# Performance work log

Measured on AMD Instinct MI355X. Metric: run time of the kernel, lower is better.

Reference implementation:

```python
import jax, jax.numpy as jnp
import numpy as np

B, T, C = 4, 1024, 1024
H, D = 16, 64            # num_heads, head_size = C // H
F = 4096                 # ffwd_size
L = 4                    # num_layers
VOCAB = 64               # input_size (activity vocab)
OUT = 65                 # output_size (acts + 1 duration)
LEN = 1024               # positional table length (block_size)


def _rmsnorm(x, g):
    eps = jnp.finfo(x.dtype).eps
    return x * jax.lax.rsqrt(jnp.mean(x * x, axis=-1, keepdims=True) + eps) * g


def setup_inputs() -> dict:
    key = jax.random.key(0)
    ks = jax.random.split(key, 16)
    std = 0.02
    acts = jax.random.randint(ks[0], (B, T), 0, VOCAB, dtype=jnp.int32)
    durations = jax.random.uniform(ks[1], (B, T), dtype=jnp.float32)
    emb_table = jax.random.normal(ks[2], (VOCAB, C - 1), dtype=jnp.float32) * std
    pos_table = jax.random.normal(ks[3], (LEN, C), dtype=jnp.float32) * std
    Wq = jax.random.normal(ks[4], (L, H, C, D), dtype=jnp.float32) * std
    Wk = jax.random.normal(ks[5], (L, H, C, D), dtype=jnp.float32) * std
    Wv = jax.random.normal(ks[6], (L, H, C, D), dtype=jnp.float32) * std
    Wo = jax.random.normal(ks[7], (L, C, C), dtype=jnp.float32) * std
    bo = jnp.zeros((L, C), dtype=jnp.float32)
    W1 = jax.random.normal(ks[8], (L, C, F), dtype=jnp.float32) * std
    b1 = jnp.zeros((L, F), dtype=jnp.float32)
    W2 = jax.random.normal(ks[9], (L, F, C), dtype=jnp.float32) * std
    b2 = jnp.zeros((L, C), dtype=jnp.float32)
    g1 = jnp.ones((L, C), dtype=jnp.float32)
    g2 = jnp.ones((L, C), dtype=jnp.float32)
    lm_W = jax.random.normal(ks[10], (C, OUT), dtype=jnp.float32) * std
    lm_b = jnp.zeros((OUT,), dtype=jnp.float32)
    return dict(acts=acts, durations=durations, emb_table=emb_table, pos_table=pos_table,
                Wq=Wq, Wk=Wk, Wv=Wv, Wo=Wo, bo=bo, W1=W1, b1=b1, W2=W2, b2=b2,
                g1=g1, g2=g2, lm_W=lm_W, lm_b=lm_b)


def reference(acts, durations, emb_table, pos_table, Wq, Wk, Wv, Wo, bo,
              W1, b1, W2, b2, g1, g2, lm_W, lm_b):
    # embedding: concat(act embedding [C-1], duration scalar) -> [B, T, C]
    x = jnp.concatenate([emb_table[acts], durations[..., None]], axis=-1)
    x = x + pos_table[:T]
    tril = jnp.tril(jnp.ones((T, T), dtype=bool))
    scale = D ** -0.5
    for l in range(L):
        h = _rmsnorm(x, g1[l])
        q = jnp.einsum('btc,hcd->bhtd', h, Wq[l])
        k = jnp.einsum('btc,hcd->bhtd', h, Wk[l])
        v = jnp.einsum('btc,hcd->bhtd', h, Wv[l])
        wei = jnp.einsum('bhtd,bhsd->bhts', q, k) * scale
        wei = jnp.where(tril, wei, -jnp.inf)
        wei = jax.nn.softmax(wei, axis=-1)
        o = jnp.einsum('bhts,bhsd->bhtd', wei, v)           # [B, H, T, D]
        o = o.transpose(0, 2, 1, 3).reshape(B, T, H * D)     # concat heads
        x = x + o @ Wo[l] + bo[l]
        h2 = _rmsnorm(x, g2[l])
        x = x + jax.nn.gelu(h2 @ W1[l] + b1[l], approximate=False) @ W2[l] + b2[l]
    logits = x @ lm_W + lm_b
    acts_logits, dur = logits[..., :OUT - 1], logits[..., OUT - 1:]
    acts_log_probs = jax.nn.log_softmax(acts_logits, axis=-1)
    log_dur = jnp.log(jax.nn.sigmoid(dur))
    return jnp.concatenate([acts_log_probs, log_dur], axis=-1)
```

## Files before the change

kernel.cpp:

```cpp
#include <hip/hip_runtime.h>

#define Bq 4
#define Tq 1024
#define Cq 1024
#define Hq 16
#define Dq 64
#define Fq 4096
#define Lq 4
#define BT (Bq*Tq)

typedef __attribute__((ext_vector_type(8))) __bf16 bf16x8;
typedef __attribute__((ext_vector_type(4))) float  floatx4;

__device__ __forceinline__ unsigned short f2bf(float f) {
  unsigned int u = __builtin_bit_cast(unsigned int, f);
  u = (u + 0x7FFFu + ((u >> 16) & 1u)) >> 16;
  return (unsigned short)u;
}

__device__ __forceinline__ void gld_lds16(const void* g, void* lds) {
  __builtin_amdgcn_global_load_lds(
      (const __attribute__((address_space(1))) unsigned int*)g,
      (__attribute__((address_space(3))) unsigned int*)lds, 16, 0, 0);
}

__device__ __forceinline__ void barrier_vmcnt4() {
  asm volatile("s_waitcnt vmcnt(4)\n\ts_barrier" ::: "memory");
}

__global__ __launch_bounds__(256) void embed_kernel(
    const int* __restrict__ acts, const float* __restrict__ dur,
    const float* __restrict__ emb, const float* __restrict__ pos,
    float* __restrict__ x)
{
  int tok = blockIdx.x;
  int t = tok & (Tq-1);
  int a = acts[tok];
  const float* er = emb + (size_t)a * (Cq-1);
  const float* pr = pos + (size_t)t * Cq;
  float* xr = x + (size_t)tok * Cq;
  float dv = dur[tok];
  for (int c = threadIdx.x; c < Cq; c += 256) {
    float v = (c < Cq-1) ? er[c] : dv;
    xr[c] = v + pr[c];
  }
}

__global__ __launch_bounds__(256) void rmsnorm_kernel(
    const float* __restrict__ x, const float* __restrict__ g,
    unsigned short* __restrict__ h)
{
  int tok = blockIdx.x, tid = threadIdx.x;
  const float4* xr = (const float4*)(x + (size_t)tok * Cq);
  float4 v = xr[tid];
  float ss = v.x*v.x + v.y*v.y + v.z*v.z + v.w*v.w;
  #pragma unroll
  for (int s = 32; s >= 1; s >>= 1) ss += __shfl_xor(ss, s, 64);
  __shared__ float ws4[4];
  if ((tid & 63) == 0) ws4[tid >> 6] = ss;
  __syncthreads();
  float tot = ws4[0] + ws4[1] + ws4[2] + ws4[3];
  float r = rsqrtf(tot * (1.0f/(float)Cq) + 1.1920928955078125e-07f);
  float4 gv = ((const float4*)g)[tid];
  unsigned short o4[4] = { f2bf(v.x*r*gv.x), f2bf(v.y*r*gv.y),
                           f2bf(v.z*r*gv.z), f2bf(v.w*r*gv.w) };
  *(uint2*)(h + (size_t)tok*Cq + tid*4) = *(const uint2*)o4;
}

__global__ void prep_layer_kernel(
    const float* __restrict__ Wq, const float* __restrict__ Wk,
    const float* __restrict__ Wv, const float* __restrict__ Wo,
    const float* __restrict__ W1, const float* __restrict__ W2,
    unsigned short* __restrict__ wqkvl, unsigned short* __restrict__ wol,
    unsigned short* __restrict__ w1l,   unsigned short* __restrict__ w2l)
{
  __shared__ float tile[32][33];
  int z = blockIdx.x;
  const float* in; unsigned short* out;
  int R, Cc, tx, ty;
  if (z < 3072) {
    int i = z >> 10, t = z & 1023;
    int hh = t >> 6, rem = t & 63;
    ty = rem >> 1; tx = rem & 1;
    const float* w = (i == 0) ? Wq : (i == 1) ? Wk : Wv;
    in = w + (size_t)hh * Cq * Dq;
    out = wqkvl + (size_t)i * 1024 * 1024 + (size_t)hh * 64 * 1024;
    R = 1024; Cc = 64;
  } else if (z < 4096) {
    int t = z - 3072;
    tx = t & 31; ty = t >> 5;
    in = Wo; out = wol; R = 1024; Cc = 1024;
  } else if (z < 8192) {
    int t = z - 4096;
    tx = t & 127; ty = t >> 7;
    in = W1; out = w1l; R = 1024; Cc = 4096;
  } else {
    int t = z - 8192;
    tx = t & 31; ty = t >> 5;
    in = W2; out = w2l; R = 4096; Cc = 1024;
  }
  int c0 = tx * 32, r0 = ty * 32;
  int lx = threadIdx.x, ly = threadIdx.y;
  #pragma unroll
  for (int i = 0; i < 32; i += 8)
    tile[ly+i][lx] = in[(size_t)(r0+ly+i)*Cc + c0 + lx];
  __syncthreads();
  #pragma unroll
  for (int i = 0; i < 32; i += 8)
    out[(size_t)(c0+ly+i)*R + r0 + lx] = f2bf(tile[lx][ly+i]);
}

template <int EPI>
__global__ __launch_bounds__(256)
void gemm_bt_kernel(const unsigned short* __restrict__ A, int lda,
                    const unsigned short* __restrict__ Bt, int ldb,
                    int KS,
                    unsigned short* __restrict__ outB, int ldc,
                    unsigned short* __restrict__ vT,
                    float* __restrict__ outF, int ldf,
                    const float* __restrict__ bias)
{
  __shared__ unsigned short lds_a[3*4096];
  __shared__ unsigned short lds_b[3*4096];
  int tid = threadIdx.x;
  int lane = tid & 63, wv = tid >> 6;
  int lane15 = lane & 15, laneh = lane >> 4;
  int m0 = blockIdx.y * 128, n0 = blockIdx.x * 128;
  int wm = wv & 1, wn = wv >> 1;

  floatx4 acc[4][4];
  #pragma unroll
  for (int i = 0; i < 4; i++)
    #pragma unroll
    for (int j = 0; j < 4; j++) acc[i][j] = (floatx4){0.f,0.f,0.f,0.f};

  int seg0 = (wv*2+0)*64 + lane;
  int seg1 = (wv*2+1)*64 + lane;
  int ra0 = seg0 >> 2, ca0 = ((seg0 & 3) ^ (ra0 & 3)) * 8;
  int ra1 = seg1 >> 2, ca1 = ((seg1 & 3) ^ (ra1 & 3)) * 8;
  const unsigned short* a_src0 = A  + (size_t)(m0+ra0)*lda + ca0;
  const unsigned short* a_src1 = A  + (size_t)(m0+ra1)*lda + ca1;
  const unsigned short* b_src0 = Bt + (size_t)(n0+ra0)*ldb + ca0;
  const unsigned short* b_src1 = Bt + (size_t)(n0+ra1)*ldb + ca1;
  unsigned short* a_dst0 = &lds_a[(wv*2+0)*512];
  unsigned short* a_dst1 = &lds_a[(wv*2+1)*512];
  unsigned short* b_dst0 = &lds_b[(wv*2+0)*512];
  unsigned short* b_dst1 = &lds_b[(wv*2+1)*512];

  int sx = (laneh ^ (lane15 & 3)) * 8;

  int kbeg = (EPI == 3) ? blockIdx.z * KS : 0;
  int nIter = KS >> 5;

  auto stage = [&](int k0, int buf) {
    int off = buf * 4096;
    gld_lds16(a_src0 + k0, a_dst0 + off);
    gld_lds16(a_src1 + k0, a_dst1 + off);
    gld_lds16(b_src0 + k0, b_dst0 + off);
    gld_lds16(b_src1 + k0, b_dst1 + off);
  };

  stage(kbeg, 0);
  stage(kbeg + 32, 1);
  int cb = 0, pb = 2;
  for (int it = 0; it < nIter; ++it) {
    barrier_vmcnt4();
    if (it + 2 < nIter) stage(kbeg + (it+2)*32, pb);
    const unsigned short* la = &lds_a[cb*4096];
    const unsigned short* lb = &lds_b[cb*4096];
    bf16x8 af[4], bf[4];
    #pragma unroll
    for (int i = 0; i < 4; i++)
      af[i] = *(const bf16x8*)&la[(wm*64 + i*16 + lane15)*32 + sx];
    #pragma unroll
    for (int j = 0; j < 4; j++)
      bf[j] = *(const bf16x8*)&lb[(wn*64 + j*16 + lane15)*32 + sx];
    #pragma unroll
    for (int i = 0; i < 4; i++)
      #pragma unroll
      for (int j = 0; j < 4; j++)
        acc[i][j] = __builtin_amdgcn_mfma_f32_16x16x32_bf16(af[i], bf[j], acc[i][j], 0, 0, 0);
    cb = (cb == 2) ? 0 : cb + 1;
    pb = (pb == 2) ? 0 : pb + 1;
  }

  float* outFz = (EPI == 3) ? outF + (size_t)blockIdx.z * BT * Cq : outF;

  #pragma unroll
  for (int i = 0; i < 4; i++) {
    int row = m0 + wm*64 + i*16 + laneh*4;
    #pragma unroll
    for (int j = 0; j < 4; j++) {
      int col = n0 + wn*64 + j*16 + lane15;
      #pragma unroll
      for (int r = 0; r < 4; r++) {
        float v = acc[i][j][r];
        int rr = row + r;
        if constexpr (EPI == 0) {
          if (col < 2048) {
            outB[(size_t)rr*ldc + col] = f2bf(v);
          } else {
            int b = rr >> 10, t = rr & (Tq-1);
            int hd = col - 2048, hh = hd >> 6, d = hd & 63;
            vT[(((size_t)b*Hq + hh)*Dq + d)*Tq + t] = f2bf(v);
          }
        } else if constexpr (EPI == 1) {
          float z = v + bias[col];
          float u = 0.79788456080286536f * (z + 0.044715f * z*z*z);
          float t = 1.f - 2.f / (__expf(2.f*u) + 1.f);
          float gl = 0.5f * z * (1.f + t);
          outB[(size_t)rr*ldc + col] = f2bf(gl);
        } else if constexpr (EPI == 2) {
          outF[(size_t)rr*ldf + col] += v + bias[col];
        } else {
          outFz[(size_t)rr*ldf + col] = v;
        }
      }
    }
  }
}

__global__ __launch_bounds__(256) void splitk_reduce_kernel(
    const float* __restrict__ p, float* __restrict__ x,
    const float* __restrict__ bias)
{
  size_t o = ((size_t)blockIdx.x * 256 + threadIdx.x) * 4;
  float4 a = *(const float4*)(p + o);
  float4 b = *(const float4*)(p + (size_t)BT*Cq + o);
  float4 xv = *(const float4*)(x + o);
  float4 bi = *(const float4*)(bias + (o & (Cq-1)));
  xv.x += a.x + b.x + bi.x;
  xv.y += a.y + b.y + bi.y;
  xv.z += a.z + b.z + bi.z;
  xv.w += a.w + b.w + bi.w;
  *(float4*)(x + o) = xv;
}

__global__ __launch_bounds__(256)
void attn_kernel(const unsigned short* __restrict__ qk,
                 const unsigned short* __restrict__ vT,
                 unsigned short* __restrict__ ob)
{
  __shared__ unsigned short Ks [2][64*64];
  __shared__ unsigned short Vts[2][64*64];
  __shared__ unsigned short Ps [4*16*64];
  int tid = threadIdx.x, lane = tid & 63, wv = tid >> 6;
  int lane15 = lane & 15, laneh = lane >> 4;
  int blk = blockIdx.x;
  int p = blk & 7, bh = blk >> 3;
  int h = bh & (Hq-1), b = bh >> 4;
  size_t tokbase = (size_t)b * Tq;
  const unsigned short* Kbase = qk + tokbase*2048 + 1024 + h*64;
  const unsigned short* Vbase = vT + (size_t)bh * Dq * Tq;

  int so  = (laneh ^ (lane15 & 7)) * 8;
  int so32 = so ^ 32;
  unsigned short* Pw = &Ps[wv*1024];

  auto stage = [&](int j0, int buf) {
    #pragma unroll
    for (int i = 0; i < 2; i++) {
      int seg = (wv*2+i)*64 + lane;
      int row = seg >> 3;
      int col = ((seg & 7) ^ (row & 7)) * 8;
      gld_lds16(Kbase + (size_t)(j0+row)*2048 + col, &Ks [buf][(wv*2+i)*512]);
      gld_lds16(Vbase + (size_t)row*Tq + j0 + col,   &Vts[buf][(wv*2+i)*512]);
    }
  };

  for (int phase = 0; phase < 2; ++phase) {
    int qt = phase ? (15 - p) : p;
    int qrow0 = qt*64 + wv*16;
    bf16x8 qf0, qf1;
    {
      const unsigned short* qp = qk + (tokbase + qrow0 + lane15)*2048 + h*64 + laneh*8;
      qf0 = *(const bf16x8*)(qp);
      qf1 = *(const bf16x8*)(qp + 32);
    }
    floatx4 oacc[4];
    #pragma unroll
    for (int d = 0; d < 4; d++) oacc[d] = (floatx4){0.f,0.f,0.f,0.f};
    float mrow = -__builtin_inff(), lrow = 0.f;
    int nT = qt + 1;

    __syncthreads();
    stage(0, 0);
    for (int it = 0; it < nT; ++it) {
      __syncthreads();
      if (it + 1 < nT) stage((it+1)*64, (it+1) & 1);
      int buf = it & 1;
      int j0 = it*64;

      floatx4 sac[4];
      #pragma unroll
      for (int jt = 0; jt < 4; jt++) {
        int row = jt*16 + lane15;
        bf16x8 kf0 = *(const bf16x8*)&Ks[buf][row*64 + so];
        bf16x8 kf1 = *(const bf16x8*)&Ks[buf][row*64 + so32];
        sac[jt] = (floatx4){0.f,0.f,0.f,0.f};
        sac[jt] = __builtin_amdgcn_mfma_f32_16x16x32_bf16(kf0, qf0, sac[jt], 0, 0, 0);
        sac[jt] = __builtin_amdgcn_mfma_f32_16x16x32_bf16(kf1, qf1, sac[jt], 0, 0, 0);
      }
      if (j0 + 63 > qrow0) {
        int tokg = qrow0 + lane15;
        #pragma unroll
        for (int jt = 0; jt < 4; jt++)
          #pragma unroll
          for (int r = 0; r < 4; r++) {
            int kv = j0 + jt*16 + laneh*4 + r;
            sac[jt][r] = (kv <= tokg) ? sac[jt][r] * 0.125f : -__builtin_inff();
          }
      } else {
        #pragma unroll
        for (int jt = 0; jt < 4; jt++)
          #pragma unroll
          for (int r = 0; r < 4; r++) sac[jt][r] *= 0.125f;
      }
      float mx = sac[0][0];
      #pragma unroll
      for (int jt = 0; jt < 4; jt++)
        #pragma unroll
        for (int r = 0; r < 4; r++) mx = fmaxf(mx, sac[jt][r]);
      mx = fmaxf(mx, __shfl_xor(mx, 16, 64));
      mx = fmaxf(mx, __shfl_xor(mx, 32, 64));
      float mn = fmaxf(mrow, mx);
      float alpha = __expf(mrow - mn);
      float psum = 0.f;
      #pragma unroll
      for (int jt = 0; jt < 4; jt++)
        #pragma unroll
        for (int r = 0; r < 4; r++) {
          float pv = __expf(sac[jt][r] - mn);
          sac[jt][r] = pv;
          psum += pv;
        }
      psum += __shfl_xor(psum, 16, 64);
      psum += __shfl_xor(psum, 32, 64);
      lrow = lrow * alpha + psum;
      mrow = mn;
      #pragma unroll
      for (int dt = 0; dt < 4; dt++)
        #pragma unroll
        for (int r = 0; r < 4; r++) oacc[dt][r] *= alpha;

      #pragma unroll
      for (int jt = 0; jt < 4; jt++) {
        unsigned int p0 = (unsigned int)f2bf(sac[jt][0]) | ((unsigned int)f2bf(sac[jt][1]) << 16);
        unsigned int p1 = (unsigned int)f2bf(sac[jt][2]) | ((unsigned int)f2bf(sac[jt][3]) << 16);
        int slot = (jt*2 + (laneh >> 1)) ^ (lane15 & 7);
        *(uint2*)&Pw[lane15*64 + slot*8 + (laneh & 1)*4] = make_uint2(p0, p1);
      }
      bf16x8 pf0 = *(const bf16x8*)&Pw[lane15*64 + so];
      bf16x8 pf1 = *(const bf16x8*)&Pw[lane15*64 + so32];
      #pragma unroll
      for (int dt = 0; dt < 4; dt++) {
        int row = dt*16 + lane15;
        bf16x8 vf0 = *(const bf16x8*)&Vts[buf][row*64 + so];
        bf16x8 vf1 = *(const bf16x8*)&Vts[buf][row*64 + so32];
        oacc[dt] = __builtin_amdgcn_mfma_f32_16x16x32_bf16(vf0, pf0, oacc[dt], 0, 0, 0);
        oacc[dt] = __builtin_amdgcn_mfma_f32_16x16x32_bf16(vf1, pf1, oacc[dt], 0, 0, 0);
      }
    }
    float inv = 1.f / lrow;
    unsigned short* orow = ob + (tokbase + qrow0 + lane15)*Cq + h*64 + laneh*4;
    #pragma unroll
    for (int dt = 0; dt < 4; dt++) {
      unsigned int u0 = (unsigned int)f2bf(oacc[dt][0]*inv) | ((unsigned int)f2bf(oacc[dt][1]*inv) << 16);
      unsigned int u1 = (unsigned int)f2bf(oacc[dt][2]*inv) | ((unsigned int)f2bf(oacc[dt][3]*inv) << 16);
      *(uint2*)&orow[dt*16] = make_uint2(u0, u1);
    }
  }
}

__global__ __launch_bounds__(256) void lmw_prep_kernel(
    const float* __restrict__ lmW, unsigned short* __restrict__ lmWt,
    float* __restrict__ lmWcol)
{
  int idx = blockIdx.x * 256 + threadIdx.x;
  int n = idx & 63, k = idx >> 6;
  lmWt[(size_t)n*Cq + k] = f2bf(lmW[(size_t)k*65 + n]);
  if (idx < Cq) lmWcol[idx] = lmW[(size_t)idx*65 + 64];
}

__global__ __launch_bounds__(64) void head_mfma_kernel(
    const float* __restrict__ x, const unsigned short* __restrict__ lmWt,
    const float* __restrict__ lmWcol, const float* __restrict__ lmb,
    float* __restrict__ out)
{
  int lane = threadIdx.x;
  int lane15 = lane & 15, laneh = lane >> 4;
  int tok0 = blockIdx.x * 16;

  floatx4 acc[4];
  #pragma unroll
  for (int jt = 0; jt < 4; jt++) acc[jt] = (floatx4){0.f,0.f,0.f,0.f};

  const float* xrow = x + (size_t)(tok0 + lane15) * Cq + laneh*8;
  const unsigned short* brow = lmWt + (size_t)lane15 * Cq + laneh*8;

  for (int k0 = 0; k0 < Cq; k0 += 32) {
    float4 a0 = *(const float4*)(xrow + k0);
    float4 a1 = *(const float4*)(xrow + k0 + 4);
    bf16x8 af;
    af[0] = (__bf16)a0.x; af[1] = (__bf16)a0.y; af[2] = (__bf16)a0.z; af[3] = (__bf16)a0.w;
    af[4] = (__bf16)a1.x; af[5] = (__bf16)a1.y; af[6] = (__bf16)a1.z; af[7] = (__bf16)a1.w;
    #pragma unroll
    for (int jt = 0; jt < 4; jt++) {
      bf16x8 bfv = *(const bf16x8*)(brow + (size_t)jt*16*Cq + k0);
      acc[jt] = __builtin_amdgcn_mfma_f32_16x16x32_bf16(af, bfv, acc[jt], 0, 0, 0);
    }
  }
  #pragma unroll
  for (int jt = 0; jt < 4; jt++) {
    float bias = lmb[jt*16 + lane15];
    #pragma unroll
    for (int r = 0; r < 4; r++) acc[jt][r] += bias;
  }
  #pragma unroll
  for (int r = 0; r < 4; r++) {
    float m = fmaxf(fmaxf(acc[0][r], acc[1][r]), fmaxf(acc[2][r], acc[3][r]));
    #pragma unroll
    for (int s = 1; s < 16; s <<= 1) m = fmaxf(m, __shfl_xor(m, s, 64));
    float se = 0.f;
    #pragma unroll
    for (int jt = 0; jt < 4; jt++) se += expf(acc[jt][r] - m);
    #pragma unroll
    for (int s = 1; s < 16; s <<= 1) se += __shfl_xor(se, s, 64);
    float lse = m + logf(se);
    int tok = tok0 + laneh*4 + r;
    float* orow = out + (size_t)tok * 65;
    #pragma unroll
    for (int jt = 0; jt < 4; jt++)
      orow[jt*16 + lane15] = acc[jt][r] - lse;
  }
  int t = lane >> 2, kq = (lane & 3) * 256;
  const float* xr2 = x + (size_t)(tok0 + t) * Cq + kq;
  const float* wc = lmWcol + kq;
  float s = 0.f;
  #pragma unroll 4
  for (int i = 0; i < 256; i += 4) {
    float4 xv = *(const float4*)(xr2 + i);
    float4 wv = *(const float4*)(wc + i);
    s += xv.x*wv.x + xv.y*wv.y + xv.z*wv.z + xv.w*wv.w;
  }
  s += __shfl_xor(s, 1, 64);
  s += __shfl_xor(s, 2, 64);
  if ((lane & 3) == 0) {
    float z = s + lmb[64];
    float ls = (z >= 0.f) ? -log1pf(expf(-z)) : (z - log1pf(expf(z)));
    out[(size_t)(tok0 + t) * 65 + 64] = ls;
  }
}

extern "C" void kernel_launch(void* const* d_in, const int* in_sizes, int n_in,
                              void* d_out, int out_size, void* d_ws, size_t ws_size,
                              hipStream_t stream) {
  const int*   acts = (const int*)  d_in[0];
  const float* dur  = (const float*)d_in[1];
  const float* emb  = (const float*)d_in[2];
  const float* pos  = (const float*)d_in[3];
  const float* Wq   = (const float*)d_in[4];
  const float* Wk   = (const float*)d_in[5];
  const float* Wv   = (const float*)d_in[6];
  const float* Wo   = (const float*)d_in[7];
  const float* bo   = (const float*)d_in[8];
  const float* W1   = (const float*)d_in[9];
  const float* b1   = (const float*)d_in[10];
  const float* W2   = (const float*)d_in[11];
  const float* b2   = (const float*)d_in[12];
  const float* g1   = (const float*)d_in[13];
  const float* g2   = (const float*)d_in[14];
  const float* lmW  = (const float*)d_in[15];
  const float* lmb  = (const float*)d_in[16];
  float* out = (float*)d_out;
  (void)in_sizes; (void)n_in; (void)out_size; (void)ws_size;

  char* w = (char*)d_ws;
  auto take = [&](size_t bytes) { char* p = w; w += (bytes + 255) & ~(size_t)255; return p; };
  unsigned short* qk  = (unsigned short*)take((size_t)BT*2048*2);
  unsigned short* vT  = (unsigned short*)take((size_t)Bq*Hq*Dq*Tq*2);
  unsigned short* ob  = (unsigned short*)take((size_t)BT*Cq*2);
  unsigned short* m1  = qk;
  unsigned short* hb  = (unsigned short*)take((size_t)BT*Cq*2);
  float*          x   = (float*)take((size_t)BT*Cq*4);
  unsigned short* wqkvl = (unsigned short*)take((size_t)3072*Cq*2);
  unsigned short* wol   = (unsigned short*)take((size_t)Cq*Cq*2);
  unsigned short* w1l   = (unsigned short*)take((size_t)Fq*Cq*2);
  unsigned short* w2l   = (unsigned short*)take((size_t)Cq*Fq*2);
  unsigned short* lmWt  = (unsigned short*)take((size_t)64*Cq*2);
  float*          lmWcol= (float*)take((size_t)Cq*4);
  float*          part  = (float*)take((size_t)2*BT*Cq*4);

  dim3 tb(32, 8);
  embed_kernel<<<BT, 256, 0, stream>>>(acts, dur, emb, pos, x);
  lmw_prep_kernel<<<256, 256, 0, stream>>>(lmW, lmWt, lmWcol);

  for (int l = 0; l < Lq; l++) {
    prep_layer_kernel<<<12288, tb, 0, stream>>>(
        Wq + (size_t)l*Hq*Cq*Dq, Wk + (size_t)l*Hq*Cq*Dq, Wv + (size_t)l*Hq*Cq*Dq,
        Wo + (size_t)l*Cq*Cq, W1 + (size_t)l*Cq*Fq, W2 + (size_t)l*Fq*Cq,
        wqkvl, wol, w1l, w2l);

    rmsnorm_kernel<<<BT, 256, 0, stream>>>(x, g1 + l*Cq, hb);
    gemm_bt_kernel<0><<<dim3(24,32), 256, 0, stream>>>(
        hb, Cq, wqkvl, Cq, Cq, qk, 2048, vT, nullptr, 0, nullptr);
    attn_kernel<<<Bq*Hq*8, 256, 0, stream>>>(qk, vT, ob);
    gemm_bt_kernel<2><<<dim3(8,32), 256, 0, stream>>>(
        ob, Cq, wol, Cq, Cq, nullptr, 0, nullptr, x, Cq, bo + l*Cq);
    rmsnorm_kernel<<<BT, 256, 0, stream>>>(x, g2 + l*Cq, hb);
    gemm_bt_kernel<1><<<dim3(32,32), 256, 0, stream>>>(
        hb, Cq, w1l, Cq, Cq, m1, Fq, nullptr, nullptr, 0, b1 + l*Fq);
    gemm_bt_kernel<3><<<dim3(8,32,2), 256, 0, stream>>>(
        m1, Fq, w2l, Fq, 2048, nullptr, 0, nullptr, part, Cq, nullptr);
    splitk_reduce_kernel<<<BT*Cq/1024, 256, 0, stream>>>(part, x, b2 + l*Cq);
  }
  head_mfma_kernel<<<BT/16, 64, 0, stream>>>(x, lmWt, lmWcol, lmb, out);
}
```

Measured before the change: 1.220 ms.

## Add 256x256-tile 8-wave pipelined GEMM for QKV and FFN-up projections

Adds a new GEMM kernel that uses 256x256 output tiles and 512 threads, double-buffered LDS staged through direct global-to-LDS loads. The K loop is split into four quarter-phases that interleave MFMA work with the next tile's loads, using fine-grained barriers, s_setprio, and an XCD-aware workgroup remap. It replaces the older GEMM for the QKV and W1+GELU projections to raise data reuse per tile and hide memory latency. In exchange it uses 128KB of LDS and many accumulator registers, and the QKV and FFN-up GEMMs now launch only 192 and 256 workgroups.

```diff
diff --git a/kernel.cpp b/kernel.cpp
--- a/kernel.cpp
+++ b/kernel.cpp
@@ -26,6 +26,19 @@
 
 __device__ __forceinline__ void barrier_vmcnt4() {
   asm volatile("s_waitcnt vmcnt(4)\n\ts_barrier" ::: "memory");
+}
+
+__device__ __forceinline__ void bar() {
+  asm volatile("s_barrier" ::: "memory");
+}
+__device__ __forceinline__ void bar_lgkm() {
+  asm volatile("s_waitcnt lgkmcnt(0)\n\ts_barrier" ::: "memory");
+}
+__device__ __forceinline__ void bar_vm6() {
+  asm volatile("s_waitcnt vmcnt(6)\n\ts_barrier" ::: "memory");
+}
+__device__ __forceinline__ void bar_vm0() {
+  asm volatile("s_waitcnt vmcnt(0)\n\ts_barrier" ::: "memory");
 }
 
 __global__ __launch_bounds__(256) void embed_kernel(
@@ -220,6 +233,187 @@
   }
 }
 
+template <int EPI>
+__global__ __launch_bounds__(512, 2)
+void gemm256_kernel(const unsigned short* __restrict__ A, int lda,
+                    const unsigned short* __restrict__ Bt, int ldb,
+                    int KS,
+                    unsigned short* __restrict__ outB, int ldc,
+                    unsigned short* __restrict__ vT,
+                    const float* __restrict__ bias)
+{
+  __shared__ unsigned short lds_a[2][256*64];
+  __shared__ unsigned short lds_b[2][256*64];
+  const int tid = threadIdx.x;
+  const int lane = tid & 63, wv = tid >> 6;
+  const int lane15 = lane & 15, laneh = lane >> 4;
+  const int wm = wv & 1, wn = wv >> 1;
+
+  const int gx = gridDim.x, gy = gridDim.y;
+  const int nwg = gx * gy;
+  int wg = (int)blockIdx.y * gx + (int)blockIdx.x;
+  if ((nwg & 7) == 0) wg = (wg & 7) * (nwg >> 3) + (wg >> 3);
+  const int tn = wg % gx;
+  const int tm = wg / gx;
+  const int m0 = tm * 256, n0 = tn * 256;
+  const int nT = KS >> 6;
+
+  const int rowS = tid >> 3;
+  const int gsw  = ((tid & 7) ^ (rowS & 7)) * 8;
+  const unsigned short* a_src = A  + (size_t)(m0 + rowS) * lda + gsw;
+  const unsigned short* b_src = Bt + (size_t)(n0 + rowS) * ldb + gsw;
+
+  auto stageA_lo = [&](int t, int b) {
+    const unsigned short* s = a_src + t*64;
+    gld_lds16(s,                    &lds_a[b][    0 + wv*512]);
+    gld_lds16(s + (size_t)64*lda,   &lds_a[b][ 4096 + wv*512]);
+  };
+  auto stageA_hi = [&](int t, int b) {
+    const unsigned short* s = a_src + t*64 + (size_t)128*lda;
+    gld_lds16(s,                    &lds_a[b][ 8192 + wv*512]);
+    gld_lds16(s + (size_t)64*lda,   &lds_a[b][12288 + wv*512]);
+  };
+  auto stageB_lo = [&](int t, int b) {
+    const unsigned short* s = b_src + t*64;
+    gld_lds16(s,                    &lds_b[b][    0 + wv*512]);
+    gld_lds16(s + (size_t)64*ldb,   &lds_b[b][ 4096 + wv*512]);
+  };
+  auto stageB_hi = [&](int t, int b) {
+    const unsigned short* s = b_src + t*64 + (size_t)128*ldb;
+    gld_lds16(s,                    &lds_b[b][ 8192 + wv*512]);
+    gld_lds16(s + (size_t)64*ldb,   &lds_b[b][12288 + wv*512]);
+  };
+
+  const int soff0 = ((laneh)     ^ (lane15 & 7)) * 8;
+  const int soff1 = ((4 + laneh) ^ (lane15 & 7)) * 8;
+  const int arow = (wm*16 + lane15) * 64;
+  const int brow = (wn*16 + lane15) * 64;
+
+  floatx4 acc[8][4];
+  #pragma unroll
+  for (int i = 0; i < 8; i++)
+    #pragma unroll
+    for (int j = 0; j < 4; j++) acc[i][j] = (floatx4){0.f,0.f,0.f,0.f};
+
+  bf16x8 af[4][2], bfr[2][2];
+
+  stageA_lo(0,0); stageB_lo(0,0); stageA_hi(0,0); stageB_hi(0,0);
+  if (nT > 1) { stageA_lo(1,1); stageB_hi(1,1); stageA_hi(1,1); }
+  bar_vm6();
+
+  for (int t = 0; t < nT; ++t) {
+    const int buf = t & 1;
+    const unsigned short* la = &lds_a[buf][0];
+    const unsigned short* lb = &lds_b[buf][0];
+
+    #pragma unroll
+    for (int ii = 0; ii < 4; ii++) {
+      af[ii][0] = *(const bf16x8*)&la[arow + ii*2048 + soff0];
+      af[ii][1] = *(const bf16x8*)&la[arow + ii*2048 + soff1];
+    }
+    #pragma unroll
+    for (int jj = 0; jj < 2; jj++) {
+      bfr[jj][0] = *(const bf16x8*)&lb[brow + jj*4096 + soff0];
+      bfr[jj][1] = *(const bf16x8*)&lb[brow + jj*4096 + soff1];
+    }
+    if (t + 1 < nT) stageB_lo(t+1, buf^1);
+    bar();
+    __builtin_amdgcn_s_setprio(1);
+    #pragma unroll
+    for (int ks = 0; ks < 2; ks++)
+      #pragma unroll
+      for (int ii = 0; ii < 4; ii++)
+        #pragma unroll
+        for (int jj = 0; jj < 2; jj++)
+          acc[ii][jj] = __builtin_amdgcn_mfma_f32_16x16x32_bf16(af[ii][ks], bfr[jj][ks], acc[ii][jj], 0, 0, 0);
+    __builtin_amdgcn_s_setprio(0);
+    bar_lgkm();
+
+    #pragma unroll
+    for (int jj = 0; jj < 2; jj++) {
+      bfr[jj][0] = *(const bf16x8*)&lb[8192 + brow + jj*4096 + soff0];
+      bfr[jj][1] = *(const bf16x8*)&lb[8192 + brow + jj*4096 + soff1];
+    }
+    if (t + 2 < nT) stageA_lo(t+2, buf);
+    bar();
+    __builtin_amdgcn_s_setprio(1);
+    #pragma unroll
+    for (int ks = 0; ks < 2; ks++)
+      #pragma unroll
+      for (int ii = 0; ii < 4; ii++)
+        #pragma unroll
+        for (int jj = 0; jj < 2; jj++)
+          acc[ii][2+jj] = __builtin_amdgcn_mfma_f32_16x16x32_bf16(af[ii][ks], bfr[jj][ks], acc[ii][2+jj], 0, 0, 0);
+    __builtin_amdgcn_s_setprio(0);
+    bar_lgkm();
+
+    #pragma unroll
+    for (int ii = 0; ii < 4; ii++) {
+      af[ii][0] = *(const bf16x8*)&la[8192 + arow + ii*2048 + soff0];
+      af[ii][1] = *(const bf16x8*)&la[8192 + arow + ii*2048 + soff1];
+    }
+    if (t + 2 < nT) stageB_hi(t+2, buf);
+    bar();
+    __builtin_amdgcn_s_setprio(1);
+    #pragma unroll
+    for (int ks = 0; ks < 2; ks++)
+      #pragma unroll
+      for (int ii = 0; ii < 4; ii++)
+        #pragma unroll
+        for (int jj = 0; jj < 2; jj++)
+          acc[4+ii][2+jj] = __builtin_amdgcn_mfma_f32_16x16x32_bf16(af[ii][ks], bfr[jj][ks], acc[4+ii][2+jj], 0, 0, 0);
+    __builtin_amdgcn_s_setprio(0);
+    bar_lgkm();
+
+    #pragma unroll
+    for (int jj = 0; jj < 2; jj++) {
+      bfr[jj][0] = *(const bf16x8*)&lb[brow + jj*4096 + soff0];
+      bfr[jj][1] = *(const bf16x8*)&lb[brow + jj*4096 + soff1];
+    }
+    if (t + 2 < nT) stageA_hi(t+2, buf);
+    if (t < nT - 2) bar_vm6(); else bar_vm0();
+    __builtin_amdgcn_s_setprio(1);
+    #pragma unroll
+    for (int ks = 0; ks < 2; ks++)
+      #pragma unroll
+      for (int ii = 0; ii < 4; ii++)
+        #pragma unroll
+        for (int jj = 0; jj < 2; jj++)
+          acc[4+ii][jj] = __builtin_amdgcn_mfma_f32_16x16x32_bf16(af[ii][ks], bfr[jj][ks], acc[4+ii][jj], 0, 0, 0);
+    __builtin_amdgcn_s_setprio(0);
+    bar_lgkm();
+  }
+
+  #pragma unroll
+  for (int i = 0; i < 8; i++) {
+    int row = m0 + (i>>2)*128 + (i&3)*32 + wm*16 + laneh*4;
+    #pragma unroll
+    for (int j = 0; j < 4; j++) {
+      int col = n0 + (j>>1)*128 + (j&1)*64 + wn*16 + lane15;
+      #pragma unroll
+      for (int r = 0; r < 4; r++) {
+        float v = acc[i][j][r];
+        int rr = row + r;
+        if constexpr (EPI == 0) {
+          if (col < 2048) {
+            outB[(size_t)rr*ldc + col] = f2bf(v);
+          } else {
+            int b = rr >> 10, t = rr & (Tq-1);
+            int hd = col - 2048, hh = hd >> 6, d = hd & 63;
+            vT[(((size_t)b*Hq + hh)*Dq + d)*Tq + t] = f2bf(v);
+          }
+        } else {
+          float z = v + bias[col];
+          float u = 0.79788456080286536f * (z + 0.044715f * z*z*z);
+          float tt = 1.f - 2.f / (__expf(2.f*u) + 1.f);
+          float gl = 0.5f * z * (1.f + tt);
+          outB[(size_t)rr*ldc + col] = f2bf(gl);
+        }
+      }
+    }
+  }
+}
+
 __global__ __launch_bounds__(256) void splitk_reduce_kernel(
     const float* __restrict__ p, float* __restrict__ x,
     const float* __restrict__ bias)
@@ -502,14 +696,14 @@
         wqkvl, wol, w1l, w2l);
 
     rmsnorm_kernel<<<BT, 256, 0, stream>>>(x, g1 + l*Cq, hb);
-    gemm_bt_kernel<0><<<dim3(24,32), 256, 0, stream>>>(
-        hb, Cq, wqkvl, Cq, Cq, qk, 2048, vT, nullptr, 0, nullptr);
+    gemm256_kernel<0><<<dim3(12,16), 512, 0, stream>>>(
+        hb, Cq, wqkvl, Cq, Cq, qk, 2048, vT, nullptr);
     attn_kernel<<<Bq*Hq*8, 256, 0, stream>>>(qk, vT, ob);
     gemm_bt_kernel<2><<<dim3(8,32), 256, 0, stream>>>(
         ob, Cq, wol, Cq, Cq, nullptr, 0, nullptr, x, Cq, bo + l*Cq);
     rmsnorm_kernel<<<BT, 256, 0, stream>>>(x, g2 + l*Cq, hb);
-    gemm_bt_kernel<1><<<dim3(32,32), 256, 0, stream>>>(
-        hb, Cq, w1l, Cq, Cq, m1, Fq, nullptr, nullptr, 0, b1 + l*Fq);
+    gemm256_kernel<1><<<dim3(16,16), 512, 0, stream>>>(
+        hb, Cq, w1l, Cq, Cq, m1, Fq, nullptr, b1 + l*Fq);
     gemm_bt_kernel<3><<<dim3(8,32,2), 256, 0, stream>>>(
         m1, Fq, w2l, Fq, 2048, nullptr, 0, nullptr, part, Cq, nullptr);
     splitk_reduce_kernel<<<BT*Cq/1024, 256, 0, stream>>>(part, x, b2 + l*Cq);
```

New measurement: 1.255 ms. 1.03x slower.
